# Kernel tuning notes

Hardware: AMD Instinct MI355X
Metric: run time of the kernel (lower is better)

Reference implementation:

```python
import jax, jax.numpy as jnp
import numpy as np
import math

B, S, D = 4, 2048, 768
H = 12
DH = D // H  # 64
NEG = -1e10

def setup_inputs() -> dict:
    key = jax.random.key(0)
    ks = jax.random.split(key, 8)
    scale = 0.02
    return {
        "hidden_states": jax.random.normal(ks[0], (B, S, D), dtype=jnp.float32),
        "attention_mask": jnp.zeros((B, 1, 1, S), dtype=jnp.float32),
        "Wq": jax.random.normal(ks[1], (D, D), dtype=jnp.float32) * scale,
        "bq": jnp.zeros((D,), dtype=jnp.float32),
        "Wk": jax.random.normal(ks[2], (D, D), dtype=jnp.float32) * scale,
        "bk": jnp.zeros((D,), dtype=jnp.float32),
        "Wv": jax.random.normal(ks[3], (D, D), dtype=jnp.float32) * scale,
        "bv": jnp.zeros((D,), dtype=jnp.float32),
    }

def reference(hidden_states, attention_mask, Wq, bq, Wk, bk, Wv, bv):
    # Linear projections; note attention_mask is accepted but unused, matching the torch module.
    def split_heads(x):  # [B,S,D] -> [B,H,S,DH]
        return x.reshape(B, S, H, DH).transpose(0, 2, 1, 3)
    q = split_heads(hidden_states @ Wq + bq)
    k = split_heads(hidden_states @ Wk + bk)
    v = split_heads(hidden_states @ Wv + bv)
    scores = jnp.einsum("bhqd,bhkd->bhqk", q, k) / math.sqrt(DH)
    causal = jnp.tril(jnp.ones((S, S), dtype=bool))  # masked_fill(mask==0, -1e10)
    scores = jnp.where(causal, scores, NEG)
    probs = jax.nn.softmax(scores, axis=-1)
    # dropout prob = 0.0 (eval) -> identity
    ctx = jnp.einsum("bhqk,bhkd->bhqd", probs, v)
    return ctx.transpose(0, 2, 1, 3).reshape(B, S, D)
```

## Files before the change

kernel.cpp:

```cpp
#include <hip/hip_runtime.h>
#include <hip/hip_bf16.h>

#define B_  4
#define S_  2048
#define D_  768
#define H_  12
#define DH_ 64

typedef __bf16 bf16;
typedef __attribute__((ext_vector_type(8))) __bf16 bf16x8;
typedef __attribute__((ext_vector_type(4))) __bf16 bf16x4;
typedef __attribute__((ext_vector_type(4))) float floatx4;
typedef __attribute__((ext_vector_type(4))) short short4v;

#if defined(__has_builtin)
#if __has_builtin(__builtin_amdgcn_mfma_f32_16x16x16bf16_1k)
#define HAVE_MFMA16_BUILTIN 1
#endif
#endif
static __device__ __forceinline__ floatx4 mfma16(short4v a, short4v b, floatx4 c) {
#ifdef HAVE_MFMA16_BUILTIN
    return __builtin_amdgcn_mfma_f32_16x16x16bf16_1k(a, b, c, 0, 0, 0);
#else
    floatx4 d = c;
    asm("v_mfma_f32_16x16x16_bf16 %0, %1, %2, %0" : "+v"(d) : "v"(a), "v"(b));
    return d;
#endif
}

__device__ __forceinline__ int swz(int row, int col) {
    return row * 64 + (col ^ ((row & 7) << 3));
}

__device__ __forceinline__ int chunk_off(int qt) {
    if (qt < 8)  return qt;
    if (qt < 16) return 8 + 2 * (qt - 8);
    if (qt < 24) return 24 + 3 * (qt - 16);
    return 48 + 4 * (qt - 24);
}

__global__ __launch_bounds__(256) void cvt_f32_bf16(const float* __restrict__ in,
                                                    bf16* __restrict__ out, int n4) {
    int i = blockIdx.x * 256 + threadIdx.x;
    if (i < n4) {
        float4 v = ((const float4*)in)[i];
        bf16x4 o;
        o[0] = (bf16)v.x; o[1] = (bf16)v.y; o[2] = (bf16)v.z; o[3] = (bf16)v.w;
        *(bf16x4*)(out + (size_t)i * 4) = o;
    }
}

__global__ __launch_bounds__(256) void w_transpose(const float* __restrict__ w0,
                                                   const float* __restrict__ w1,
                                                   const float* __restrict__ w2,
                                                   bf16* __restrict__ Wt)
{
    const int which = blockIdx.z;
    const float* W = (which == 0) ? w0 : (which == 1 ? w1 : w2);
    bf16* dst = Wt + (size_t)which * D_ * D_;
    __shared__ bf16 t[64 * 72];
    const int k0 = blockIdx.x * 64, n0 = blockIdx.y * 64;
    const int tid = threadIdx.x;
    {
        int r = tid >> 2;
        int c0 = (tid & 3) * 16;
        #pragma unroll
        for (int q = 0; q < 4; q++) {
            float4 v = *(const float4*)(W + (size_t)(k0 + r) * D_ + n0 + c0 + q * 4);
            t[(c0 + q * 4 + 0) * 72 + r] = (bf16)v.x;
            t[(c0 + q * 4 + 1) * 72 + r] = (bf16)v.y;
            t[(c0 + q * 4 + 2) * 72 + r] = (bf16)v.z;
            t[(c0 + q * 4 + 3) * 72 + r] = (bf16)v.w;
        }
    }
    __syncthreads();
    {
        int n = tid >> 3, seg = tid & 7;
        *(bf16x8*)(dst + (size_t)(n0 + n) * D_ + k0 + seg * 8) =
            *(const bf16x8*)(t + n * 72 + seg * 8);
        *(bf16x8*)(dst + (size_t)(n0 + n + 32) * D_ + k0 + seg * 8) =
            *(const bf16x8*)(t + (n + 32) * 72 + seg * 8);
    }
}

__global__ __launch_bounds__(256) void qkv_gemm(
    const bf16* __restrict__ Xb, const bf16* __restrict__ Wt,
    const float* __restrict__ bq, const float* __restrict__ bk,
    const float* __restrict__ bv, bf16* __restrict__ QKV)
{
    const int which = blockIdx.z;
    const bf16* Wm = Wt + (size_t)which * D_ * D_;
    const float* bias = (which == 0) ? bq : (which == 1 ? bk : bv);
    bf16* out = QKV + (size_t)which * B_ * H_ * S_ * DH_;

    __shared__ bf16 As[128 * 72];
    __shared__ bf16 Bs[128 * 72];

    const int tid  = threadIdx.x;
    const int wave = tid >> 6, lane = tid & 63;
    const int wr = wave >> 1, wc = wave & 1;
    const int g = lane >> 4, ln = lane & 15;
    const int m0 = blockIdx.x * 128, n0 = blockIdx.y * 128;

    floatx4 acc[4][4];
    #pragma unroll
    for (int i = 0; i < 4; i++)
        #pragma unroll
        for (int j = 0; j < 4; j++)
            acc[i][j] = (floatx4){0.f, 0.f, 0.f, 0.f};

    int row_[4], seg_[4];
    #pragma unroll
    for (int t = 0; t < 4; t++) { int fc = tid + t * 256; row_[t] = fc >> 3; seg_[t] = fc & 7; }

    bf16x8 apf[4], bpf[4];
    #pragma unroll
    for (int t = 0; t < 4; t++) {
        apf[t] = *(const bf16x8*)(Xb + (size_t)(m0 + row_[t]) * D_ + seg_[t] * 8);
        bpf[t] = *(const bf16x8*)(Wm + (size_t)(n0 + row_[t]) * D_ + seg_[t] * 8);
    }

    for (int k0 = 0; k0 < D_; k0 += 64) {
        __syncthreads();
        #pragma unroll
        for (int t = 0; t < 4; t++) {
            *(bf16x8*)(As + row_[t] * 72 + seg_[t] * 8) = apf[t];
            *(bf16x8*)(Bs + row_[t] * 72 + seg_[t] * 8) = bpf[t];
        }
        __syncthreads();
        if (k0 + 64 < D_) {
            #pragma unroll
            for (int t = 0; t < 4; t++) {
                apf[t] = *(const bf16x8*)(Xb + (size_t)(m0 + row_[t]) * D_ + k0 + 64 + seg_[t] * 8);
                bpf[t] = *(const bf16x8*)(Wm + (size_t)(n0 + row_[t]) * D_ + k0 + 64 + seg_[t] * 8);
            }
        }
        #pragma unroll
        for (int ks = 0; ks < 2; ks++) {
            bf16x8 af[4], bfr[4];
            #pragma unroll
            for (int i = 0; i < 4; i++)
                af[i] = *(const bf16x8*)(As + (wr * 64 + i * 16 + ln) * 72 + ks * 32 + g * 8);
            #pragma unroll
            for (int j = 0; j < 4; j++)
                bfr[j] = *(const bf16x8*)(Bs + (wc * 64 + j * 16 + ln) * 72 + ks * 32 + g * 8);
            #pragma unroll
            for (int i = 0; i < 4; i++)
                #pragma unroll
                for (int j = 0; j < 4; j++)
                    acc[i][j] = __builtin_amdgcn_mfma_f32_16x16x32_bf16(af[i], bfr[j], acc[i][j], 0, 0, 0);
        }
    }

    #pragma unroll
    for (int i = 0; i < 4; i++) {
        #pragma unroll
        for (int j = 0; j < 4; j++) {
            int col = n0 + wc * 64 + j * 16 + ln;
            float bv_ = bias[col];
            int h = col >> 6, dh = col & 63;
            int rowbase = m0 + wr * 64 + i * 16 + g * 4;
            int b = rowbase >> 11, s0 = rowbase & 2047;
            if (which == 2) {
                bf16x4 o;
                #pragma unroll
                for (int r = 0; r < 4; r++) o[r] = (bf16)(acc[i][j][r] + bv_);
                *(bf16x4*)(out + ((size_t)((b * H_ + h) * DH_ + dh)) * S_ + s0) = o;
            } else {
                #pragma unroll
                for (int r = 0; r < 4; r++)
                    out[(((size_t)(b * H_ + h) * S_ + s0 + r) << 6) + dh] =
                        (bf16)(acc[i][j][r] + bv_);
            }
        }
    }
}

__global__ __launch_bounds__(256, 4) void attn_chunk(const bf16* __restrict__ QKV,
                                                     float* __restrict__ out,
                                                     bf16* __restrict__ Opart,
                                                     float* __restrict__ Lpart)
{
    const int cid = 79 - blockIdx.x;
    const int bh = blockIdx.y;
    const int b = bh / H_, h = bh % H_;

    int qt, c;
    if (cid < 8)       { qt = cid; c = 0; }
    else if (cid < 24) { qt = 8 + ((cid - 8) >> 1); c = (cid - 8) & 1; }
    else if (cid < 48) { int t3 = cid - 24; qt = 16 + t3 / 3; c = t3 - (qt - 16) * 3; }
    else               { int t4 = cid - 48; qt = 24 + (t4 >> 2); c = t4 & 3; }
    const int nch = (qt >> 3) + 1;
    const int kt0 = c * 8;
    const int kt1 = min(kt0 + 7, qt);

    const size_t MAT = (size_t)B_ * H_ * S_ * DH_;
    const bf16* Q  = QKV +           (size_t)bh * S_ * DH_;
    const bf16* K  = QKV + MAT +     (size_t)bh * S_ * DH_;
    const bf16* Vt = QKV + 2 * MAT + (size_t)bh * S_ * DH_;

    __shared__ bf16 Ks[64 * 64];
    __shared__ bf16 Vts[64 * 64];

    const int tid  = threadIdx.x;
    const int wave = tid >> 6, lane = tid & 63;
    const int g = lane >> 4, ln = lane & 15;
    const int srow = tid >> 3, sseg = tid & 7;

    bf16x8 qf[2];
    {
        const bf16* qrow = Q + (size_t)(qt * 64 + wave * 16 + ln) * DH_;
        qf[0] = *(const bf16x8*)(qrow + g * 8);
        qf[1] = *(const bf16x8*)(qrow + 32 + g * 8);
    }

    const short4v ones16 = {0x3F80, 0x3F80, 0x3F80, 0x3F80};

    floatx4 accO[4];
    #pragma unroll
    for (int dt = 0; dt < 4; dt++) accO[dt] = (floatx4){0.f, 0.f, 0.f, 0.f};
    floatx4 accL = (floatx4){0.f, 0.f, 0.f, 0.f};

    const bf16* kptr = K  + (size_t)(kt0 * 64 + srow) * DH_ + sseg * 8;
    const bf16* vptr = Vt + (size_t)srow * S_ + kt0 * 64 + sseg * 8;

    bf16x8 ka = *(const bf16x8*)kptr;
    bf16x8 kb = *(const bf16x8*)(kptr + 32 * DH_);
    bf16x8 va = *(const bf16x8*)vptr;
    bf16x8 vb = *(const bf16x8*)(vptr + (size_t)32 * S_);

    for (int kt = kt0; kt <= kt1; ++kt) {
        __syncthreads();
        *(bf16x8*)(Ks  + swz(srow, sseg * 8)) = ka;
        *(bf16x8*)(Ks  + swz(srow + 32, sseg * 8)) = kb;
        *(bf16x8*)(Vts + swz(srow, sseg * 8)) = va;
        *(bf16x8*)(Vts + swz(srow + 32, sseg * 8)) = vb;
        __syncthreads();
        if (kt < kt1) {
            kptr += 64 * DH_;
            vptr += 64;
            ka = *(const bf16x8*)kptr;
            kb = *(const bf16x8*)(kptr + 32 * DH_);
            va = *(const bf16x8*)vptr;
            vb = *(const bf16x8*)(vptr + (size_t)32 * S_);
        }

        __builtin_amdgcn_s_setprio(1);
        #pragma unroll
        for (int j = 0; j < 4; j++) {
            floatx4 accS = (floatx4){0.f, 0.f, 0.f, 0.f};
            #pragma unroll
            for (int cc = 0; cc < 2; cc++) {
                bf16x8 kf = *(const bf16x8*)(Ks + swz(j * 16 + ln, cc * 32 + g * 8));
                accS = __builtin_amdgcn_mfma_f32_16x16x32_bf16(kf, qf[cc], accS, 0, 0, 0);
            }

            #pragma unroll
            for (int r = 0; r < 4; r++) accS[r] = __expf(accS[r] * 0.125f);
            if (kt == qt) {
                const int krow = j * 16 + g * 4;
                const int qrow = wave * 16 + ln;
                #pragma unroll
                for (int r = 0; r < 4; r++)
                    if (krow + r > qrow) accS[r] = 0.f;
            }

            bf16x4 pa;
            #pragma unroll
            for (int r = 0; r < 4; r++) pa[r] = (bf16)accS[r];
            short4v pas = __builtin_bit_cast(short4v, pa);

            accL = mfma16(pas, ones16, accL);

            #pragma unroll
            for (int dt = 0; dt < 4; dt++) {
                short4v vf = *(const short4v*)(Vts + swz(dt * 16 + ln, j * 16 + g * 4));
                accO[dt] = mfma16(pas, vf, accO[dt]);
            }
        }
        __builtin_amdgcn_s_setprio(0);
    }

    if (nch == 1) {
        float inv[4];
        #pragma unroll
        for (int r = 0; r < 4; r++) inv[r] = 1.0f / accL[r];
        #pragma unroll
        for (int dt = 0; dt < 4; dt++) {
            int dh = dt * 16 + ln;
            #pragma unroll
            for (int r = 0; r < 4; r++) {
                int q = qt * 64 + wave * 16 + g * 4 + r;
                out[((size_t)(b * S_ + q)) * D_ + h * DH_ + dh] = accO[dt][r] * inv[r];
            }
        }
    } else {
        const int chunk = bh * 80 + chunk_off(qt) + c;
        bf16x8 p0, p1;
        #pragma unroll
        for (int e = 0; e < 8; e++) {
            p0[e] = (bf16)accO[e >> 2][e & 3];
            p1[e] = (bf16)accO[2 + (e >> 2)][e & 3];
        }
        bf16* dst = Opart + (size_t)chunk * 4096 + tid * 16;
        *(bf16x8*)dst = p0;
        *(bf16x8*)(dst + 8) = p1;
        if (ln == 0) {
            #pragma unroll
            for (int r = 0; r < 4; r++)
                Lpart[chunk * 64 + wave * 16 + g * 4 + r] = accL[r];
        }
    }
}

__global__ __launch_bounds__(256) void attn_reduce(const bf16* __restrict__ Opart,
                                                   const float* __restrict__ Lpart,
                                                   float* __restrict__ out)
{
    const int qt = 8 + blockIdx.x;
    const int bh = blockIdx.y;
    const int b = bh / H_, h = bh % H_;
    const int nch = (qt >> 3) + 1;
    const int cb = bh * 80 + chunk_off(qt);

    const int tid  = threadIdx.x;
    const int wave = tid >> 6, lane = tid & 63;
    const int g = lane >> 4, ln = lane & 15;

    float o[16];
    #pragma unroll
    for (int e = 0; e < 16; e++) o[e] = 0.f;
    float ls[4] = {0.f, 0.f, 0.f, 0.f};

    for (int cidx = 0; cidx < nch; cidx++) {
        const bf16* p = Opart + (size_t)(cb + cidx) * 4096 + tid * 16;
        bf16x8 v0 = *(const bf16x8*)p;
        bf16x8 v1 = *(const bf16x8*)(p + 8);
        #pragma unroll
        for (int e = 0; e < 8; e++) { o[e] += (float)v0[e]; o[8 + e] += (float)v1[e]; }
        #pragma unroll
        for (int r = 0; r < 4; r++)
            ls[r] += Lpart[(cb + cidx) * 64 + wave * 16 + g * 4 + r];
    }
    float inv[4];
    #pragma unroll
    for (int r = 0; r < 4; r++) inv[r] = 1.0f / ls[r];
    #pragma unroll
    for (int j = 0; j < 4; j++) {
        int dh = j * 16 + ln;
        #pragma unroll
        for (int r = 0; r < 4; r++) {
            int q = qt * 64 + wave * 16 + g * 4 + r;
            out[((size_t)(b * S_ + q)) * D_ + h * DH_ + dh] = o[j * 4 + r] * inv[r];
        }
    }
}

extern "C" void kernel_launch(void* const* d_in, const int* in_sizes, int n_in,
                              void* d_out, int out_size, void* d_ws, size_t ws_size,
                              hipStream_t stream) {
    const float* hs = (const float*)d_in[0];
    const float* Wq = (const float*)d_in[2];
    const float* bq = (const float*)d_in[3];
    const float* Wk = (const float*)d_in[4];
    const float* bk = (const float*)d_in[5];
    const float* Wv = (const float*)d_in[6];
    const float* bv = (const float*)d_in[7];
    float* out = (float*)d_out;

    bf16* Xb    = (bf16*)d_ws;
    bf16* Wt    = Xb + (size_t)8192 * 768;
    bf16* QKV   = Wt + (size_t)3 * 768 * 768;
    bf16* Opart = QKV + (size_t)3 * B_ * H_ * S_ * DH_;
    float* Lpart = (float*)(Opart + (size_t)3840 * 4096);

    cvt_f32_bf16<<<6144, 256, 0, stream>>>(hs, Xb, 1572864);
    w_transpose<<<dim3(12, 12, 3), 256, 0, stream>>>(Wq, Wk, Wv, Wt);
    qkv_gemm<<<dim3(64, 6, 3), 256, 0, stream>>>(Xb, Wt, bq, bk, bv, QKV);
    attn_chunk<<<dim3(80, 48), 256, 0, stream>>>(QKV, out, Opart, Lpart);
    attn_reduce<<<dim3(24, 48), 256, 0, stream>>>(Opart, Lpart, out);
}
```

Before: 196.3 us.

## Double-buffer K/V LDS tiles in attention and fuse prep kernels

Attention K/V tiles now alternate between two LDS buffers. The next tile is written after computing on the current one, so each iteration needs one barrier instead of two. The fp32-to-bf16 conversion of the hidden states and the weight transpose are merged into one kernel to save a launch. LDS use per block doubles, which could reduce occupancy.

```diff
diff --git a/kernel.cpp b/kernel.cpp
--- a/kernel.cpp
+++ b/kernel.cpp
@@ -39,28 +39,30 @@
     return 48 + 4 * (qt - 24);
 }
 
-__global__ __launch_bounds__(256) void cvt_f32_bf16(const float* __restrict__ in,
-                                                    bf16* __restrict__ out, int n4) {
-    int i = blockIdx.x * 256 + threadIdx.x;
-    if (i < n4) {
-        float4 v = ((const float4*)in)[i];
+__global__ __launch_bounds__(256) void prep(const float* __restrict__ hs,
+                                            const float* __restrict__ w0,
+                                            const float* __restrict__ w1,
+                                            const float* __restrict__ w2,
+                                            bf16* __restrict__ Xb,
+                                            bf16* __restrict__ Wt)
+{
+    __shared__ bf16 t[64 * 72];
+    const int bid = blockIdx.x;
+    const int tid = threadIdx.x;
+    if (bid < 6144) {
+        int i = bid * 256 + tid;
+        float4 v = ((const float4*)hs)[i];
         bf16x4 o;
         o[0] = (bf16)v.x; o[1] = (bf16)v.y; o[2] = (bf16)v.z; o[3] = (bf16)v.w;
-        *(bf16x4*)(out + (size_t)i * 4) = o;
-    }
-}
-
-__global__ __launch_bounds__(256) void w_transpose(const float* __restrict__ w0,
-                                                   const float* __restrict__ w1,
-                                                   const float* __restrict__ w2,
-                                                   bf16* __restrict__ Wt)
-{
-    const int which = blockIdx.z;
+        *(bf16x4*)(Xb + (size_t)i * 4) = o;
+        return;
+    }
+    const int t4 = bid - 6144;
+    const int which = t4 / 144;
+    const int rem = t4 % 144;
     const float* W = (which == 0) ? w0 : (which == 1 ? w1 : w2);
     bf16* dst = Wt + (size_t)which * D_ * D_;
-    __shared__ bf16 t[64 * 72];
-    const int k0 = blockIdx.x * 64, n0 = blockIdx.y * 64;
-    const int tid = threadIdx.x;
+    const int k0 = (rem / 12) * 64, n0 = (rem % 12) * 64;
     {
         int r = tid >> 2;
         int c0 = (tid & 3) * 16;
@@ -199,13 +201,15 @@
     const bf16* K  = QKV + MAT +     (size_t)bh * S_ * DH_;
     const bf16* Vt = QKV + 2 * MAT + (size_t)bh * S_ * DH_;
 
-    __shared__ bf16 Ks[64 * 64];
-    __shared__ bf16 Vts[64 * 64];
+    __shared__ bf16 Ks[2][64 * 64];
+    __shared__ bf16 Vts[2][64 * 64];
 
     const int tid  = threadIdx.x;
     const int wave = tid >> 6, lane = tid & 63;
     const int g = lane >> 4, ln = lane & 15;
     const int srow = tid >> 3, sseg = tid & 7;
+    const int wofs = swz(srow, sseg * 8);
+    const int wofs2 = swz(srow + 32, sseg * 8);
 
     bf16x8 qf[2];
     {
@@ -228,13 +232,13 @@
     bf16x8 kb = *(const bf16x8*)(kptr + 32 * DH_);
     bf16x8 va = *(const bf16x8*)vptr;
     bf16x8 vb = *(const bf16x8*)(vptr + (size_t)32 * S_);
-
+    *(bf16x8*)(Ks[0]  + wofs)  = ka;
+    *(bf16x8*)(Ks[0]  + wofs2) = kb;
+    *(bf16x8*)(Vts[0] + wofs)  = va;
+    *(bf16x8*)(Vts[0] + wofs2) = vb;
+
+    int cur = 0;
     for (int kt = kt0; kt <= kt1; ++kt) {
-        __syncthreads();
-        *(bf16x8*)(Ks  + swz(srow, sseg * 8)) = ka;
-        *(bf16x8*)(Ks  + swz(srow + 32, sseg * 8)) = kb;
-        *(bf16x8*)(Vts + swz(srow, sseg * 8)) = va;
-        *(bf16x8*)(Vts + swz(srow + 32, sseg * 8)) = vb;
         __syncthreads();
         if (kt < kt1) {
             kptr += 64 * DH_;
@@ -244,6 +248,8 @@
             va = *(const bf16x8*)vptr;
             vb = *(const bf16x8*)(vptr + (size_t)32 * S_);
         }
+        const bf16* Kc = Ks[cur];
+        const bf16* Vc = Vts[cur];
 
         __builtin_amdgcn_s_setprio(1);
         #pragma unroll
@@ -251,7 +257,7 @@
             floatx4 accS = (floatx4){0.f, 0.f, 0.f, 0.f};
             #pragma unroll
             for (int cc = 0; cc < 2; cc++) {
-                bf16x8 kf = *(const bf16x8*)(Ks + swz(j * 16 + ln, cc * 32 + g * 8));
+                bf16x8 kf = *(const bf16x8*)(Kc + swz(j * 16 + ln, cc * 32 + g * 8));
                 accS = __builtin_amdgcn_mfma_f32_16x16x32_bf16(kf, qf[cc], accS, 0, 0, 0);
             }
 
@@ -274,11 +280,21 @@
 
             #pragma unroll
             for (int dt = 0; dt < 4; dt++) {
-                short4v vf = *(const short4v*)(Vts + swz(dt * 16 + ln, j * 16 + g * 4));
+                short4v vf = *(const short4v*)(Vc + swz(dt * 16 + ln, j * 16 + g * 4));
                 accO[dt] = mfma16(pas, vf, accO[dt]);
             }
         }
         __builtin_amdgcn_s_setprio(0);
+
+        if (kt < kt1) {
+            bf16* Kn = Ks[cur ^ 1];
+            bf16* Vn = Vts[cur ^ 1];
+            *(bf16x8*)(Kn + wofs)  = ka;
+            *(bf16x8*)(Kn + wofs2) = kb;
+            *(bf16x8*)(Vn + wofs)  = va;
+            *(bf16x8*)(Vn + wofs2) = vb;
+            cur ^= 1;
+        }
     }
 
     if (nch == 1) {
@@ -374,8 +390,7 @@
     bf16* Opart = QKV + (size_t)3 * B_ * H_ * S_ * DH_;
     float* Lpart = (float*)(Opart + (size_t)3840 * 4096);
 
-    cvt_f32_bf16<<<6144, 256, 0, stream>>>(hs, Xb, 1572864);
-    w_transpose<<<dim3(12, 12, 3), 256, 0, stream>>>(Wq, Wk, Wv, Wt);
+    prep<<<6576, 256, 0, stream>>>(hs, Wq, Wk, Wv, Xb, Wt);
     qkv_gemm<<<dim3(64, 6, 3), 256, 0, stream>>>(Xb, Wt, bq, bk, bv, QKV);
     attn_chunk<<<dim3(80, 48), 256, 0, stream>>>(QKV, out, Opart, Lpart);
     attn_reduce<<<dim3(24, 48), 256, 0, stream>>>(Opart, Lpart, out);
```

Measured after the change: 200.7 us. 2.2% more time.

## Merge prep kernels and load GEMM tiles directly into LDS with swizzle

Applied to the files above, without the earlier changes.

Combines the activation bf16 conversion and the weight transpose into one launch, removing one kernel launch. The QKV GEMM now uses global_load_lds to copy tiles straight into XOR-swizzled shared memory, replacing the register-staged prefetch and padded layout. This cuts register traffic and LDS footprint. The cost is that the register double-buffer prefetch is gone, so global-load latency is no longer overlapped with the MFMA work of the previous tile.

```diff
diff --git a/kernel.cpp b/kernel.cpp
--- a/kernel.cpp
+++ b/kernel.cpp
@@ -32,6 +32,12 @@
     return row * 64 + (col ^ ((row & 7) << 3));
 }
 
+__device__ __forceinline__ void gload16(const bf16* g, bf16* l) {
+    __builtin_amdgcn_global_load_lds(
+        (const __attribute__((address_space(1))) void*)g,
+        (__attribute__((address_space(3))) void*)l, 16, 0, 0);
+}
+
 __device__ __forceinline__ int chunk_off(int qt) {
     if (qt < 8)  return qt;
     if (qt < 16) return 8 + 2 * (qt - 8);
@@ -39,28 +45,30 @@
     return 48 + 4 * (qt - 24);
 }
 
-__global__ __launch_bounds__(256) void cvt_f32_bf16(const float* __restrict__ in,
-                                                    bf16* __restrict__ out, int n4) {
-    int i = blockIdx.x * 256 + threadIdx.x;
-    if (i < n4) {
-        float4 v = ((const float4*)in)[i];
+__global__ __launch_bounds__(256) void prep(const float* __restrict__ hs,
+                                            const float* __restrict__ w0,
+                                            const float* __restrict__ w1,
+                                            const float* __restrict__ w2,
+                                            bf16* __restrict__ Xb,
+                                            bf16* __restrict__ Wt)
+{
+    __shared__ bf16 t[64 * 72];
+    const int bid = blockIdx.x;
+    const int tid = threadIdx.x;
+    if (bid < 6144) {
+        int i = bid * 256 + tid;
+        float4 v = ((const float4*)hs)[i];
         bf16x4 o;
         o[0] = (bf16)v.x; o[1] = (bf16)v.y; o[2] = (bf16)v.z; o[3] = (bf16)v.w;
-        *(bf16x4*)(out + (size_t)i * 4) = o;
-    }
-}
-
-__global__ __launch_bounds__(256) void w_transpose(const float* __restrict__ w0,
-                                                   const float* __restrict__ w1,
-                                                   const float* __restrict__ w2,
-                                                   bf16* __restrict__ Wt)
-{
-    const int which = blockIdx.z;
+        *(bf16x4*)(Xb + (size_t)i * 4) = o;
+        return;
+    }
+    const int t4 = bid - 6144;
+    const int which = t4 / 144;
+    const int rem = t4 % 144;
     const float* W = (which == 0) ? w0 : (which == 1 ? w1 : w2);
     bf16* dst = Wt + (size_t)which * D_ * D_;
-    __shared__ bf16 t[64 * 72];
-    const int k0 = blockIdx.x * 64, n0 = blockIdx.y * 64;
-    const int tid = threadIdx.x;
+    const int k0 = (rem / 12) * 64, n0 = (rem % 12) * 64;
     {
         int r = tid >> 2;
         int c0 = (tid & 3) * 16;
@@ -93,8 +101,8 @@
     const float* bias = (which == 0) ? bq : (which == 1 ? bk : bv);
     bf16* out = QKV + (size_t)which * B_ * H_ * S_ * DH_;
 
-    __shared__ bf16 As[128 * 72];
-    __shared__ bf16 Bs[128 * 72];
+    __shared__ bf16 As[128 * 64];
+    __shared__ bf16 Bs[128 * 64];
 
     const int tid  = threadIdx.x;
     const int wave = tid >> 6, lane = tid & 63;
@@ -109,41 +117,36 @@
         for (int j = 0; j < 4; j++)
             acc[i][j] = (floatx4){0.f, 0.f, 0.f, 0.f};
 
-    int row_[4], seg_[4];
-    #pragma unroll
-    for (int t = 0; t < 4; t++) { int fc = tid + t * 256; row_[t] = fc >> 3; seg_[t] = fc & 7; }
-
-    bf16x8 apf[4], bpf[4];
+    int row_[4], scol_[4];
     #pragma unroll
     for (int t = 0; t < 4; t++) {
-        apf[t] = *(const bf16x8*)(Xb + (size_t)(m0 + row_[t]) * D_ + seg_[t] * 8);
-        bpf[t] = *(const bf16x8*)(Wm + (size_t)(n0 + row_[t]) * D_ + seg_[t] * 8);
+        int c = tid + t * 256;
+        row_[t]  = c >> 3;
+        scol_[t] = ((c & 7) * 8) ^ ((row_[t] & 7) << 3);
     }
 
     for (int k0 = 0; k0 < D_; k0 += 64) {
+        if (k0) __syncthreads();
+        #pragma unroll
+        for (int t = 0; t < 4; t++) {
+            bf16* ldst = As + (size_t)(t * 256 + wave * 64) * 8;
+            gload16(Xb + (size_t)(m0 + row_[t]) * D_ + k0 + scol_[t], ldst);
+        }
+        #pragma unroll
+        for (int t = 0; t < 4; t++) {
+            bf16* ldst = Bs + (size_t)(t * 256 + wave * 64) * 8;
+            gload16(Wm + (size_t)(n0 + row_[t]) * D_ + k0 + scol_[t], ldst);
+        }
         __syncthreads();
-        #pragma unroll
-        for (int t = 0; t < 4; t++) {
-            *(bf16x8*)(As + row_[t] * 72 + seg_[t] * 8) = apf[t];
-            *(bf16x8*)(Bs + row_[t] * 72 + seg_[t] * 8) = bpf[t];
-        }
-        __syncthreads();
-        if (k0 + 64 < D_) {
-            #pragma unroll
-            for (int t = 0; t < 4; t++) {
-                apf[t] = *(const bf16x8*)(Xb + (size_t)(m0 + row_[t]) * D_ + k0 + 64 + seg_[t] * 8);
-                bpf[t] = *(const bf16x8*)(Wm + (size_t)(n0 + row_[t]) * D_ + k0 + 64 + seg_[t] * 8);
-            }
-        }
         #pragma unroll
         for (int ks = 0; ks < 2; ks++) {
             bf16x8 af[4], bfr[4];
             #pragma unroll
             for (int i = 0; i < 4; i++)
-                af[i] = *(const bf16x8*)(As + (wr * 64 + i * 16 + ln) * 72 + ks * 32 + g * 8);
+                af[i] = *(const bf16x8*)(As + swz(wr * 64 + i * 16 + ln, ks * 32 + g * 8));
             #pragma unroll
             for (int j = 0; j < 4; j++)
-                bfr[j] = *(const bf16x8*)(Bs + (wc * 64 + j * 16 + ln) * 72 + ks * 32 + g * 8);
+                bfr[j] = *(const bf16x8*)(Bs + swz(wc * 64 + j * 16 + ln, ks * 32 + g * 8));
             #pragma unroll
             for (int i = 0; i < 4; i++)
                 #pragma unroll
@@ -374,8 +377,7 @@
     bf16* Opart = QKV + (size_t)3 * B_ * H_ * S_ * DH_;
     float* Lpart = (float*)(Opart + (size_t)3840 * 4096);
 
-    cvt_f32_bf16<<<6144, 256, 0, stream>>>(hs, Xb, 1572864);
-    w_transpose<<<dim3(12, 12, 3), 256, 0, stream>>>(Wq, Wk, Wv, Wt);
+    prep<<<6576, 256, 0, stream>>>(hs, Wq, Wk, Wv, Xb, Wt);
     qkv_gemm<<<dim3(64, 6, 3), 256, 0, stream>>>(Xb, Wt, bq, bk, bv, QKV);
     attn_chunk<<<dim3(80, 48), 256, 0, stream>>>(QKV, out, Opart, Lpart);
     attn_reduce<<<dim3(24, 48), 256, 0, stream>>>(Opart, Lpart, out);
```

Result: faster. 189.9 us (-3.3%).
